# Optimization experiments

Hardware: AMD Instinct MI355X
Metric: run time of the kernel (lower is better)

The kernel has to match this reference:

```python
import jax, jax.numpy as jnp
import numpy as np

N = 100000   # nodes
E = 1600000  # edges
HID = 128    # hidden_dim
H = 8        # heads
C = HID // H # head_dim = out_channels per head


def setup_inputs() -> dict:
    key = jax.random.key(0)
    ks = jax.random.split(key, 10)
    x = jax.random.normal(ks[0], (N, HID), jnp.float32)
    edge_index = jax.random.randint(ks[1], (2, E), 0, N, dtype=jnp.int64)
    edge_attr = jax.random.uniform(ks[2], (E,), jnp.float32)
    # GATConv params (lin_src == lin_dst shared since in_channels is int)
    W = jax.random.normal(ks[3], (HID, H * C), jnp.float32) / np.sqrt(HID)
    att_src = jax.random.normal(ks[4], (H, C), jnp.float32) / np.sqrt(C)
    att_dst = jax.random.normal(ks[5], (H, C), jnp.float32) / np.sqrt(C)
    # lin_edge: Linear(edge_dim=1, H*C, bias=False) -> weight [H*C, 1] stored as [H, C]
    w_edge = jax.random.normal(ks[6], (H, C), jnp.float32)
    att_edge = jax.random.normal(ks[7], (H, C), jnp.float32) / np.sqrt(C)
    bias = jnp.zeros((H * C,), jnp.float32)
    gamma = jnp.ones((HID,), jnp.float32)
    beta = jnp.zeros((HID,), jnp.float32)
    return dict(x=x, edge_index=edge_index, edge_attr=edge_attr, W=W,
                att_src=att_src, att_dst=att_dst, w_edge=w_edge,
                att_edge=att_edge, bias=bias, gamma=gamma, beta=beta)


def reference(x, edge_index, edge_attr, W, att_src, att_dst, w_edge, att_edge, bias, gamma, beta):
    n = x.shape[0]
    src, dst = edge_index[0], edge_index[1]
    # add_self_loops with fill_value='mean': loop edge_attr = per-dst-node mean of edge_attr
    ones = jnp.ones_like(edge_attr)
    deg = jax.ops.segment_sum(ones, dst, num_segments=n)
    loop_attr = jax.ops.segment_sum(edge_attr, dst, num_segments=n) / jnp.maximum(deg, 1.0)
    ar = jnp.arange(n, dtype=src.dtype)
    src = jnp.concatenate([src, ar])
    dst = jnp.concatenate([dst, ar])
    ea = jnp.concatenate([edge_attr, loop_attr])  # [E+N]

    h = (x @ W).reshape(n, H, C)                  # [N,H,C]
    a_src = (h * att_src).sum(-1)                 # [N,H]
    a_dst = (h * att_dst).sum(-1)                 # [N,H]
    # edge_dim=1: alpha_edge = <lin_edge(ea), att_edge> = ea * sum(w_edge*att_edge)
    w_e = (w_edge * att_edge).sum(-1)             # [H]
    alpha = a_src[src] + a_dst[dst] + ea[:, None] * w_e  # [E+N, H]
    alpha = jax.nn.leaky_relu(alpha, 0.2)
    # segment softmax over incoming edges of each dst node (all nodes have a self-loop)
    m = jax.ops.segment_max(alpha, dst, num_segments=n)      # [N,H]
    ex = jnp.exp(alpha - m[dst])
    denom = jax.ops.segment_sum(ex, dst, num_segments=n)     # [N,H]
    p = ex / (denom[dst] + 1e-16)
    # scatter-aggregate weighted messages, concat heads, bias
    out = jax.ops.segment_sum(p[:, :, None] * h[src], dst, num_segments=n)
    out = out.reshape(n, H * C) + bias
    # residual + LayerNorm + ReLU
    y = out + x
    mu = y.mean(-1, keepdims=True)
    var = ((y - mu) ** 2).mean(-1, keepdims=True)
    y = (y - mu) * jax.lax.rsqrt(var + 1e-5) * gamma + beta
    return jax.nn.relu(y)
```

## Files before the change

kernel.cpp:

```cpp
#include <hip/hip_runtime.h>
#include <math.h>

#define HID 128
#define HEADS 8
#define CDIM 16
#define NB1 256

typedef short bf8 __attribute__((ext_vector_type(8)));
typedef float f32x4 __attribute__((ext_vector_type(4)));

__device__ __forceinline__ unsigned short f2bf(float f) {
    unsigned u = __float_as_uint(f);
    unsigned r = (u + 0x7fffu + ((u >> 16) & 1u)) >> 16;
    return (unsigned short)r;
}
__device__ __forceinline__ float bf2f(unsigned short u) {
    return __uint_as_float(((unsigned)u) << 16);
}

__global__ __launch_bounds__(256) void k_tw(const float* __restrict__ W,
                                            unsigned short* __restrict__ Wt) {
    int idx = blockIdx.x * 256 + threadIdx.x;
    int j = idx >> 7, k = idx & 127;
    Wt[idx] = f2bf(W[k * HID + j]);
}

__global__ __launch_bounds__(256) void k_hist(const int* __restrict__ dst,
                                              int* __restrict__ cntmat,
                                              int E, int per, int nbkt) {
    __shared__ int h[256];
    int t = threadIdx.x;
    h[t] = 0;
    __syncthreads();
    int b0 = blockIdx.x * per;
    int b1 = min(b0 + per, E);
    for (int e = b0 + t; e < b1; e += 256)
        atomicAdd(&h[dst[e] >> 9], 1);
    __syncthreads();
    if (t < nbkt) cntmat[t * NB1 + blockIdx.x] = h[t];
}

__global__ __launch_bounds__(256) void kscanA(const int* __restrict__ in,
                                              int* __restrict__ tmp,
                                              int* __restrict__ bsum, int M) {
    __shared__ int lds[256];
    int t = threadIdx.x;
    int base = blockIdx.x * 1024 + t * 4;
    int v[4];
#pragma unroll
    for (int i = 0; i < 4; i++) {
        int idx = base + i;
        v[i] = (idx < M) ? in[idx] : 0;
    }
    int s = v[0] + v[1] + v[2] + v[3];
    lds[t] = s;
    __syncthreads();
    for (int off = 1; off < 256; off <<= 1) {
        int xv = (t >= off) ? lds[t - off] : 0;
        __syncthreads();
        lds[t] += xv;
        __syncthreads();
    }
    int run = (t > 0) ? lds[t - 1] : 0;
#pragma unroll
    for (int i = 0; i < 4; i++) {
        int idx = base + i;
        if (idx < M) tmp[idx] = run;
        run += v[i];
    }
    if (t == 255) bsum[blockIdx.x] = lds[255];
}

__global__ __launch_bounds__(128) void kscanB(const int* __restrict__ bsum,
                                              int* __restrict__ bscan, int nb,
                                              const float* __restrict__ w_edge,
                                              const float* __restrict__ att_edge,
                                              float* __restrict__ w_e) {
    __shared__ int lds[128];
    int t = threadIdx.x;
    if (t < HEADS) {
        float s = 0.f;
        for (int c = 0; c < CDIM; c++) s += w_edge[t * CDIM + c] * att_edge[t * CDIM + c];
        w_e[t] = s;
    }
    lds[t] = (t < nb) ? bsum[t] : 0;
    __syncthreads();
    for (int off = 1; off < 128; off <<= 1) {
        int xv = (t >= off) ? lds[t - off] : 0;
        __syncthreads();
        lds[t] += xv;
        __syncthreads();
    }
    bscan[t] = (t > 0) ? lds[t - 1] : 0;
}

__global__ __launch_bounds__(256) void kscanC(const int* __restrict__ tmp,
                                              const int* __restrict__ bscan,
                                              int* __restrict__ ofs, int M) {
    int i = blockIdx.x * 256 + threadIdx.x;
    if (i < M) ofs[i] = tmp[i] + bscan[i >> 10];
}

__global__ __launch_bounds__(256) void k_scat(const int* __restrict__ src,
                                              const int* __restrict__ dst,
                                              const float* __restrict__ eattr,
                                              const int* __restrict__ ofs,
                                              int* __restrict__ d1,
                                              int2* __restrict__ erec1,
                                              int E, int per, int nbkt) {
    __shared__ int cur[256];
    int t = threadIdx.x;
    if (t < nbkt) cur[t] = ofs[t * NB1 + blockIdx.x];
    __syncthreads();
    int b0 = blockIdx.x * per;
    int b1 = min(b0 + per, E);
    for (int e = b0 + t; e < b1; e += 256) {
        int d = dst[e];
        int pos = atomicAdd(&cur[d >> 9], 1);
        d1[pos] = d;
        erec1[pos] = make_int2(src[e], __float_as_int(eattr[e]));
    }
}

__global__ __launch_bounds__(256) void k_bin(const int* __restrict__ ofs,
                                             const int* __restrict__ d1,
                                             const int2* __restrict__ erec1,
                                             int* __restrict__ row_ptr,
                                             int2* __restrict__ erec,
                                             int N, int E, int nbkt) {
    __shared__ int h2[512];
    __shared__ int s2[256];
    __shared__ int cur2[512];
    int b = blockIdx.x, t = threadIdx.x;
    int base = ofs[b * NB1];
    int end = (b + 1 < nbkt) ? ofs[(b + 1) * NB1] : E;
    h2[t] = 0; h2[t + 256] = 0;
    __syncthreads();
    for (int e = base + t; e < end; e += 256)
        atomicAdd(&h2[d1[e] & 511], 1);
    __syncthreads();
    int a0 = h2[2 * t], a1 = h2[2 * t + 1];
    s2[t] = a0 + a1;
    __syncthreads();
    for (int off = 1; off < 256; off <<= 1) {
        int v = (t >= off) ? s2[t - off] : 0;
        __syncthreads();
        s2[t] += v;
        __syncthreads();
    }
    int ex = (t > 0) ? s2[t - 1] : 0;
    int p0 = base + ex;
    int p1 = p0 + a0;
    int ng = b * 512 + 2 * t;
    if (ng <= N) row_ptr[ng] = p0;
    if (ng + 1 <= N) row_ptr[ng + 1] = p1;
    cur2[2 * t] = p0;
    cur2[2 * t + 1] = p1;
    __syncthreads();
    for (int e = base + t; e < end; e += 256) {
        int d = d1[e];
        int pos = atomicAdd(&cur2[d & 511], 1);
        erec[pos] = erec1[e];
    }
}

__global__ __launch_bounds__(256) void k_gemm(const float* __restrict__ x,
                                              const unsigned short* __restrict__ Wt,
                                              const float* __restrict__ att_src,
                                              const float* __restrict__ att_dst,
                                              unsigned short* __restrict__ hbf,
                                              float* __restrict__ a_src,
                                              float* __restrict__ a_dst, int N) {
    int tid = threadIdx.x;
    int wv = tid >> 6, lane = tid & 63;
    int nloc = lane & 15, q = lane >> 4;
    int node = blockIdx.x * 64 + wv * 16 + nloc;
    int nc = min(node, N - 1);
    const float* xp = x + (size_t)nc * HID + q * 8;
    const unsigned short* wp = Wt + nloc * HID + q * 8;
    f32x4 acc[8];
#pragma unroll
    for (int i = 0; i < 8; i++) acc[i] = (f32x4){0.f, 0.f, 0.f, 0.f};
#pragma unroll
    for (int ch = 0; ch < 4; ch++) {
        float4 xv0 = *(const float4*)(xp + ch * 32);
        float4 xv1 = *(const float4*)(xp + ch * 32 + 4);
        bf8 bfrag;
        bfrag[0] = (short)f2bf(xv0.x); bfrag[1] = (short)f2bf(xv0.y);
        bfrag[2] = (short)f2bf(xv0.z); bfrag[3] = (short)f2bf(xv0.w);
        bfrag[4] = (short)f2bf(xv1.x); bfrag[5] = (short)f2bf(xv1.y);
        bfrag[6] = (short)f2bf(xv1.z); bfrag[7] = (short)f2bf(xv1.w);
#pragma unroll
        for (int jt = 0; jt < 8; jt++) {
            bf8 afrag = *(const bf8*)(wp + (size_t)jt * 16 * HID + ch * 32);
            acc[jt] = __builtin_amdgcn_mfma_f32_16x16x32_bf16(afrag, bfrag, acc[jt], 0, 0, 0);
        }
    }
    bool ok = node < N;
    size_t hb = (size_t)nc * HID;
#pragma unroll
    for (int jt = 0; jt < 8; jt++) {
        int j0 = jt * 16 + q * 4;
        float4 as4 = *(const float4*)(att_src + j0);
        float4 ad4 = *(const float4*)(att_dst + j0);
        f32x4 a = acc[jt];
        float ps = a[0] * as4.x + a[1] * as4.y + a[2] * as4.z + a[3] * as4.w;
        float pd = a[0] * ad4.x + a[1] * ad4.y + a[2] * ad4.z + a[3] * ad4.w;
        ps += __shfl_xor(ps, 16, 64); ps += __shfl_xor(ps, 32, 64);
        pd += __shfl_xor(pd, 16, 64); pd += __shfl_xor(pd, 32, 64);
        if (ok) {
            ushort4 hv;
            hv.x = f2bf(a[0]); hv.y = f2bf(a[1]); hv.z = f2bf(a[2]); hv.w = f2bf(a[3]);
            *(ushort4*)(hbf + hb + j0) = hv;
            if (q == 0) {
                a_src[(size_t)node * 8 + jt] = ps;
                a_dst[(size_t)node * 8 + jt] = pd;
            }
        }
    }
}

__global__ __launch_bounds__(64) void k_node(const int* __restrict__ row_ptr,
                                             const int2* __restrict__ erec,
                                             const float* __restrict__ a_src,
                                             const float* __restrict__ a_dst,
                                             const float* __restrict__ w_e,
                                             const unsigned short* __restrict__ hbf,
                                             const float* __restrict__ x,
                                             const float* __restrict__ bias,
                                             const float* __restrict__ gamma,
                                             const float* __restrict__ beta,
                                             float* __restrict__ out, int N) {
    int n = blockIdx.x;
    int lane = threadIdx.x;
    int r0 = row_ptr[n], r1 = row_ptr[n + 1];
    __shared__ float lex[64][9];
    __shared__ int lsrc[64];
    __shared__ float accs[128];
    __shared__ float wl[16];

    float ad[8], we[8];
#pragma unroll
    for (int q = 0; q < 8; q++) {
        ad[q] = a_dst[(size_t)n * 8 + q];
        we[q] = w_e[q];
    }
    int sub = lane >> 4;
    int colg = lane & 15;
    int whead = colg >> 1;
    const unsigned short* hbase = hbf + (size_t)colg * 8;

    float acc[8];
#pragma unroll
    for (int j = 0; j < 8; j++) acc[j] = 0.f;
    float wsum = 0.f;
    float suma = 0.f;

    for (int base = r0; base < r1; base += 64) {
        int e = base + lane;
        if (e < r1) {
            int2 rec = erec[e];
            int s = rec.x;
            float a = __int_as_float(rec.y);
            suma += a;
            lsrc[lane] = s;
            const float* asp = a_src + (size_t)s * 8;
#pragma unroll
            for (int q = 0; q < 8; q++) {
                float v = asp[q] + ad[q] + a * we[q];
                v = v > 0.f ? v : 0.2f * v;
                lex[lane][q] = __expf(v);
            }
        } else {
            lsrc[lane] = 0;
#pragma unroll
            for (int q = 0; q < 8; q++) lex[lane][q] = 0.f;
        }
        __syncthreads();
        int nt4 = (min(64, r1 - base) + 3) >> 2;
        for (int kk = 0; kk < nt4; kk++) {
            int ke = 4 * kk + sub;
            int s = lsrc[ke];
            bf8 hv = *(const bf8*)(hbase + (size_t)s * HID);
            float w = lex[ke][whead];
            wsum += w;
#pragma unroll
            for (int j = 0; j < 8; j++)
                acc[j] = fmaf(w, bf2f((unsigned short)hv[j]), acc[j]);
        }
        __syncthreads();
    }

#pragma unroll
    for (int j = 0; j < 8; j++) {
        acc[j] += __shfl_xor(acc[j], 16, 64);
        acc[j] += __shfl_xor(acc[j], 32, 64);
    }
    wsum += __shfl_xor(wsum, 16, 64);
    wsum += __shfl_xor(wsum, 32, 64);
#pragma unroll
    for (int off = 32; off; off >>= 1) suma += __shfl_xor(suma, off, 64);

    if (lane < 16) {
#pragma unroll
        for (int j = 0; j < 8; j++) accs[lane * 8 + j] = acc[j];
        wl[lane] = wsum;
    }
    __syncthreads();

    int head = lane >> 3;
    float denom = wl[head * 2];
    float a0 = accs[2 * lane], a1 = accs[2 * lane + 1];

    int deg = r1 - r0;
    float la = suma / fmaxf((float)deg, 1.0f);
    float adh = a_dst[(size_t)n * 8 + head];
    float weh = w_e[head];
    float vs = a_src[(size_t)n * 8 + head] + adh + la * weh;
    vs = vs > 0.f ? vs : 0.2f * vs;
    float exs = __expf(vs);
    size_t bx = (size_t)n * HID;
    ushort2 hs = *(const ushort2*)(hbf + bx + 2 * lane);
    a0 = fmaf(exs, bf2f(hs.x), a0);
    a1 = fmaf(exs, bf2f(hs.y), a1);
    float inv = 1.f / (denom + exs + 1e-16f);

    float2 xv = *(const float2*)(x + bx + 2 * lane);
    float2 bv = *(const float2*)(bias + 2 * lane);
    float y0 = a0 * inv + bv.x + xv.x;
    float y1 = a1 * inv + bv.y + xv.y;
    float ss = y0 + y1, sq = y0 * y0 + y1 * y1;
#pragma unroll
    for (int off = 32; off; off >>= 1) {
        ss += __shfl_xor(ss, off, 64);
        sq += __shfl_xor(sq, off, 64);
    }
    float mu = ss * (1.f / 128.f);
    float var = sq * (1.f / 128.f) - mu * mu;
    float r = rsqrtf(fmaxf(var, 0.f) + 1e-5f);
    float2 gv = *(const float2*)(gamma + 2 * lane);
    float2 tv = *(const float2*)(beta + 2 * lane);
    float o0 = (y0 - mu) * r * gv.x + tv.x;
    float o1 = (y1 - mu) * r * gv.y + tv.y;
    float2 ov = make_float2(fmaxf(o0, 0.f), fmaxf(o1, 0.f));
    *(float2*)(out + bx + 2 * lane) = ov;
}

extern "C" void kernel_launch(void* const* d_in, const int* in_sizes, int n_in,
                              void* d_out, int out_size, void* d_ws, size_t ws_size,
                              hipStream_t stream) {
    const float* x        = (const float*)d_in[0];
    const int*   ei       = (const int*)d_in[1];
    const float* eattr    = (const float*)d_in[2];
    const float* W        = (const float*)d_in[3];
    const float* att_src  = (const float*)d_in[4];
    const float* att_dst  = (const float*)d_in[5];
    const float* w_edge   = (const float*)d_in[6];
    const float* att_edge = (const float*)d_in[7];
    const float* bias     = (const float*)d_in[8];
    const float* gamma    = (const float*)d_in[9];
    const float* beta     = (const float*)d_in[10];

    int N = in_sizes[0] / HID;
    int E = in_sizes[2];
    const int* src = ei;
    const int* dst = ei + E;
    float* out = (float*)d_out;

    int nbkt = (N + 511) >> 9;
    int M = nbkt * NB1;
    int per = (E + NB1 - 1) / NB1;

    char* ws = (char*)d_ws;
    size_t off = 0;
    auto alloc = [&](size_t bytes) { char* p = ws + off; off += (bytes + 255) & ~255ull; return p; };
    unsigned short* hbf = (unsigned short*)alloc((size_t)N * HID * 2);
    unsigned short* Wt  = (unsigned short*)alloc((size_t)HID * HID * 2);
    float* a_src   = (float*)alloc((size_t)N * 8 * 4);
    float* a_dst   = (float*)alloc((size_t)N * 8 * 4);
    int2*  erec    = (int2*) alloc((size_t)E * 8);
    int2*  erec1   = (int2*) alloc((size_t)E * 8);
    int*   d1      = (int*)  alloc((size_t)E * 4);
    int*   cntmat  = (int*)  alloc((size_t)M * 4);
    int*   stmp    = (int*)  alloc((size_t)M * 4);
    int*   ofs     = (int*)  alloc((size_t)M * 4);
    int*   bsum    = (int*)  alloc(128 * 4);
    int*   bscan   = (int*)  alloc(128 * 4);
    int*   row_ptr = (int*)  alloc((size_t)(N + 1) * 4);
    float* w_e     = (float*)alloc(8 * 4);

    int nbA = (M + 1023) / 1024;

    k_tw<<<64, 256, 0, stream>>>(W, Wt);
    k_hist<<<NB1, 256, 0, stream>>>(dst, cntmat, E, per, nbkt);
    kscanA<<<nbA, 256, 0, stream>>>(cntmat, stmp, bsum, M);
    kscanB<<<1, 128, 0, stream>>>(bsum, bscan, nbA, w_edge, att_edge, w_e);
    kscanC<<<(M + 255) / 256, 256, 0, stream>>>(stmp, bscan, ofs, M);
    k_scat<<<NB1, 256, 0, stream>>>(src, dst, eattr, ofs, d1, erec1, E, per, nbkt);
    k_bin<<<nbkt, 256, 0, stream>>>(ofs, d1, erec1, row_ptr, erec, N, E, nbkt);
    k_gemm<<<(N + 63) / 64, 256, 0, stream>>>(x, Wt, att_src, att_dst, hbf, a_src, a_dst, N);
    k_node<<<N, 64, 0, stream>>>(row_ptr, erec, a_src, a_dst, w_e, hbf, x,
                                 bias, gamma, beta, out, N);
}
```

Measured before the change: 336.2 us.

## Pack four nodes per block, drop LDS staging in node kernel, fuse scan offset

```diff
diff --git a/kernel.cpp b/kernel.cpp
--- a/kernel.cpp
+++ b/kernel.cpp
@@ -94,23 +94,20 @@
     bscan[t] = (t > 0) ? lds[t - 1] : 0;
 }
 
-__global__ __launch_bounds__(256) void kscanC(const int* __restrict__ tmp,
-                                              const int* __restrict__ bscan,
-                                              int* __restrict__ ofs, int M) {
-    int i = blockIdx.x * 256 + threadIdx.x;
-    if (i < M) ofs[i] = tmp[i] + bscan[i >> 10];
-}
-
 __global__ __launch_bounds__(256) void k_scat(const int* __restrict__ src,
                                               const int* __restrict__ dst,
                                               const float* __restrict__ eattr,
-                                              const int* __restrict__ ofs,
+                                              const int* __restrict__ tmp,
+                                              const int* __restrict__ bscan,
                                               int* __restrict__ d1,
                                               int2* __restrict__ erec1,
                                               int E, int per, int nbkt) {
     __shared__ int cur[256];
     int t = threadIdx.x;
-    if (t < nbkt) cur[t] = ofs[t * NB1 + blockIdx.x];
+    if (t < nbkt) {
+        int idx = t * NB1 + blockIdx.x;
+        cur[t] = tmp[idx] + bscan[idx >> 10];
+    }
     __syncthreads();
     int b0 = blockIdx.x * per;
     int b1 = min(b0 + per, E);
@@ -122,7 +119,8 @@
     }
 }
 
-__global__ __launch_bounds__(256) void k_bin(const int* __restrict__ ofs,
+__global__ __launch_bounds__(256) void k_bin(const int* __restrict__ tmp,
+                                             const int* __restrict__ bscan,
                                              const int* __restrict__ d1,
                                              const int2* __restrict__ erec1,
                                              int* __restrict__ row_ptr,
@@ -132,8 +130,13 @@
     __shared__ int s2[256];
     __shared__ int cur2[512];
     int b = blockIdx.x, t = threadIdx.x;
-    int base = ofs[b * NB1];
-    int end = (b + 1 < nbkt) ? ofs[(b + 1) * NB1] : E;
+    int i0 = b * NB1;
+    int base = tmp[i0] + bscan[i0 >> 10];
+    int end = E;
+    if (b + 1 < nbkt) {
+        int i1 = (b + 1) * NB1;
+        end = tmp[i1] + bscan[i1 >> 10];
+    }
     h2[t] = 0; h2[t + 256] = 0;
     __syncthreads();
     for (int e = base + t; e < end; e += 256)
@@ -220,75 +223,58 @@
     }
 }
 
-__global__ __launch_bounds__(64) void k_node(const int* __restrict__ row_ptr,
-                                             const int2* __restrict__ erec,
-                                             const float* __restrict__ a_src,
-                                             const float* __restrict__ a_dst,
-                                             const float* __restrict__ w_e,
-                                             const unsigned short* __restrict__ hbf,
-                                             const float* __restrict__ x,
-                                             const float* __restrict__ bias,
-                                             const float* __restrict__ gamma,
-                                             const float* __restrict__ beta,
-                                             float* __restrict__ out, int N) {
-    int n = blockIdx.x;
-    int lane = threadIdx.x;
+__global__ __launch_bounds__(256) void k_node(const int* __restrict__ row_ptr,
+                                              const int2* __restrict__ erec,
+                                              const float* __restrict__ a_src,
+                                              const float* __restrict__ a_dst,
+                                              const float* __restrict__ w_e,
+                                              const unsigned short* __restrict__ hbf,
+                                              const float* __restrict__ x,
+                                              const float* __restrict__ bias,
+                                              const float* __restrict__ gamma,
+                                              const float* __restrict__ beta,
+                                              float* __restrict__ out, int N) {
+    int wv = threadIdx.x >> 6;
+    int lane = threadIdx.x & 63;
+    int n = blockIdx.x * 4 + wv;
+    if (n >= N) return;
     int r0 = row_ptr[n], r1 = row_ptr[n + 1];
-    __shared__ float lex[64][9];
-    __shared__ int lsrc[64];
-    __shared__ float accs[128];
-    __shared__ float wl[16];
-
-    float ad[8], we[8];
-#pragma unroll
-    for (int q = 0; q < 8; q++) {
-        ad[q] = a_dst[(size_t)n * 8 + q];
-        we[q] = w_e[q];
-    }
     int sub = lane >> 4;
     int colg = lane & 15;
-    int whead = colg >> 1;
-    const unsigned short* hbase = hbf + (size_t)colg * 8;
+    int wh = colg >> 1;
+    float ad_h = a_dst[(size_t)n * 8 + wh];
+    float we_h = w_e[wh];
 
     float acc[8];
 #pragma unroll
     for (int j = 0; j < 8; j++) acc[j] = 0.f;
-    float wsum = 0.f;
-    float suma = 0.f;
-
-    for (int base = r0; base < r1; base += 64) {
-        int e = base + lane;
-        if (e < r1) {
-            int2 rec = erec[e];
+    float wsum = 0.f, suma = 0.f;
+
+    int e = r0 + sub;
+    if (e < r1) {
+        int2 rec = erec[e];
+        for (;;) {
+            int en = e + 4;
+            bool more = (en < r1);
+            int2 recn;
+            if (more) recn = erec[en];
             int s = rec.x;
             float a = __int_as_float(rec.y);
-            suma += a;
-            lsrc[lane] = s;
-            const float* asp = a_src + (size_t)s * 8;
-#pragma unroll
-            for (int q = 0; q < 8; q++) {
-                float v = asp[q] + ad[q] + a * we[q];
-                v = v > 0.f ? v : 0.2f * v;
-                lex[lane][q] = __expf(v);
-            }
-        } else {
-            lsrc[lane] = 0;
-#pragma unroll
-            for (int q = 0; q < 8; q++) lex[lane][q] = 0.f;
-        }
-        __syncthreads();
-        int nt4 = (min(64, r1 - base) + 3) >> 2;
-        for (int kk = 0; kk < nt4; kk++) {
-            int ke = 4 * kk + sub;
-            int s = lsrc[ke];
-            bf8 hv = *(const bf8*)(hbase + (size_t)s * HID);
-            float w = lex[ke][whead];
+            const unsigned short* hp = hbf + (size_t)s * HID + colg * 8;
+            bf8 hv = *(const bf8*)hp;
+            float asv = a_src[(size_t)s * 8 + wh];
+            float v = asv + ad_h + a * we_h;
+            v = v > 0.f ? v : 0.2f * v;
+            float w = __expf(v);
             wsum += w;
+            suma += (colg == 0) ? a : 0.f;
 #pragma unroll
             for (int j = 0; j < 8; j++)
                 acc[j] = fmaf(w, bf2f((unsigned short)hv[j]), acc[j]);
+            if (!more) break;
+            e = en;
+            rec = recn;
         }
-        __syncthreads();
     }
 
 #pragma unroll
@@ -298,22 +284,20 @@
     }
     wsum += __shfl_xor(wsum, 16, 64);
     wsum += __shfl_xor(wsum, 32, 64);
-#pragma unroll
-    for (int off = 32; off; off >>= 1) suma += __shfl_xor(suma, off, 64);
-
-    if (lane < 16) {
-#pragma unroll
-        for (int j = 0; j < 8; j++) accs[lane * 8 + j] = acc[j];
-        wl[lane] = wsum;
-    }
-    __syncthreads();
-
+    suma += __shfl_xor(suma, 16, 64);
+    suma += __shfl_xor(suma, 32, 64);
+
+    float accA = sub == 0 ? acc[0] : sub == 1 ? acc[2] : sub == 2 ? acc[4] : acc[6];
+    float accB = sub == 0 ? acc[1] : sub == 1 ? acc[3] : sub == 2 ? acc[5] : acc[7];
+    int srcL = ((lane & 3) << 4) | (lane >> 2);
+    float a0 = __shfl(accA, srcL, 64);
+    float a1 = __shfl(accB, srcL, 64);
     int head = lane >> 3;
-    float denom = wl[head * 2];
-    float a0 = accs[2 * lane], a1 = accs[2 * lane + 1];
+    float denom = __shfl(wsum, head << 1, 64);
+    float sa = __shfl(suma, 0, 64);
 
     int deg = r1 - r0;
-    float la = suma / fmaxf((float)deg, 1.0f);
+    float la = sa / fmaxf((float)deg, 1.0f);
     float adh = a_dst[(size_t)n * 8 + head];
     float weh = w_e[head];
     float vs = a_src[(size_t)n * 8 + head] + adh + la * weh;
@@ -383,7 +367,6 @@
     int*   d1      = (int*)  alloc((size_t)E * 4);
     int*   cntmat  = (int*)  alloc((size_t)M * 4);
     int*   stmp    = (int*)  alloc((size_t)M * 4);
-    int*   ofs     = (int*)  alloc((size_t)M * 4);
     int*   bsum    = (int*)  alloc(128 * 4);
     int*   bscan   = (int*)  alloc(128 * 4);
     int*   row_ptr = (int*)  alloc((size_t)(N + 1) * 4);
@@ -395,10 +378,9 @@
     k_hist<<<NB1, 256, 0, stream>>>(dst, cntmat, E, per, nbkt);
     kscanA<<<nbA, 256, 0, stream>>>(cntmat, stmp, bsum, M);
     kscanB<<<1, 128, 0, stream>>>(bsum, bscan, nbA, w_edge, att_edge, w_e);
-    kscanC<<<(M + 255) / 256, 256, 0, stream>>>(stmp, bscan, ofs, M);
-    k_scat<<<NB1, 256, 0, stream>>>(src, dst, eattr, ofs, d1, erec1, E, per, nbkt);
-    k_bin<<<nbkt, 256, 0, stream>>>(ofs, d1, erec1, row_ptr, erec, N, E, nbkt);
+    k_scat<<<NB1, 256, 0, stream>>>(src, dst, eattr, stmp, bscan, d1, erec1, E, per, nbkt);
+    k_bin<<<nbkt, 256, 0, stream>>>(stmp, bscan, d1, erec1, row_ptr, erec, N, E, nbkt);
     k_gemm<<<(N + 63) / 64, 256, 0, stream>>>(x, Wt, att_src, att_dst, hbf, a_src, a_dst, N);
-    k_node<<<N, 64, 0, stream>>>(row_ptr, erec, a_src, a_dst, w_e, hbf, x,
-                                 bias, gamma, beta, out, N);
-}
+    k_node<<<(N + 3) / 4, 256, 0, stream>>>(row_ptr, erec, a_src, a_dst, w_e, hbf, x,
+                                            bias, gamma, beta, out, N);
+}
```

Measured after the change: 335.3 us. Within noise of the previous version (-0.3%).
